# Kernel optimization log

Measured on AMD Instinct MI355X. Metric: run time of the kernel, lower is better.

Reference implementation:

```python
import jax, jax.numpy as jnp
import numpy as np

NQ = 4  # n_qubits_per_head


def _apply_ry(state, theta, q):
    # state: (N, 2,2,2,2) real amplitudes; theta: (N,) per-element angle; wire q
    st = jnp.moveaxis(state, 1 + q, -1)
    c = jnp.cos(0.5 * theta).reshape(-1, 1, 1, 1)
    s = jnp.sin(0.5 * theta).reshape(-1, 1, 1, 1)
    a0, a1 = st[..., 0], st[..., 1]
    st = jnp.stack([c * a0 - s * a1, s * a0 + c * a1], axis=-1)
    return jnp.moveaxis(st, -1, 1 + q)


def _apply_cnot(state, ctrl, tgt):
    st = jnp.moveaxis(state, (1 + ctrl, 1 + tgt), (-2, -1))
    st = jnp.stack([st[..., 0, :], st[..., 1, ::-1]], axis=-2)
    return jnp.moveaxis(st, (-2, -1), (1 + ctrl, 1 + tgt))


def _quantum_circuit(x_in, par):
    # x_in: (N, NQ) data angles; par: (N, L, NQ) variational angles (per head, tiled)
    N = x_in.shape[0]
    L = par.shape[1]
    state = jnp.zeros((N, 2, 2, 2, 2), x_in.dtype).at[:, 0, 0, 0, 0].set(1.0)
    for l in range(L):
        for q in range(NQ):
            state = _apply_ry(state, par[:, l, q], q)
        for q in range(NQ - 1):
            state = _apply_cnot(state, q, q + 1)
        state = _apply_cnot(state, NQ - 1, 0)
    for q in range(NQ):
        state = _apply_ry(state, x_in[:, q], q)
    p = state * state  # probabilities (real amplitudes: only RY/CNOT gates)
    zs = []
    for q in range(NQ):
        st = jnp.moveaxis(p, 1 + q, -1)
        zs.append(jnp.sum(st[..., 0], axis=(1, 2, 3)) - jnp.sum(st[..., 1], axis=(1, 2, 3)))
    return jnp.stack(zs, axis=-1)  # (N, NQ)


def setup_inputs() -> dict:
    key = jax.random.key(0)
    ks = jax.random.split(key, 6)
    B, T, E, H, L = 4, 2048, 1024, 16, 2
    scale = 1.0 / np.sqrt(E)
    x = jax.random.normal(ks[0], (B, T, E), dtype=jnp.float32)
    Wq = jax.random.normal(ks[1], (E, E), dtype=jnp.float32) * scale
    Wk = jax.random.normal(ks[2], (E, E), dtype=jnp.float32) * scale
    Wv = jax.random.normal(ks[3], (E, E), dtype=jnp.float32) * scale
    Wo = jax.random.normal(ks[4], (E, E), dtype=jnp.float32) * scale
    qparams = jax.random.normal(ks[5], (H, L, NQ), dtype=jnp.float32)
    return {"x": x, "Wq": Wq, "Wk": Wk, "Wv": Wv, "Wo": Wo, "qparams": qparams}


def reference(x, Wq, Wk, Wv, Wo, qparams):
    B, T, E = x.shape
    H, L, _ = qparams.shape
    hd = E // H
    q = x @ Wq.T
    k = x @ Wk.T
    v = x @ Wv.T
    # NOTE: original scales by sqrt(embed_dim), not sqrt(head_dim)
    scores = jnp.einsum('bte,bse->bts', q, k) / jnp.sqrt(jnp.asarray(E, x.dtype))
    w = jax.nn.softmax(scores, axis=-1)
    out = jnp.einsum('bts,bse->bte', w, v)
    oh = out.reshape(B, T, H, hd)
    N = B * T * H
    xin = oh[..., :NQ].reshape(N, NQ)
    par = jnp.broadcast_to(qparams[None, None], (B, T, H, L, NQ)).reshape(N, L, NQ)
    z = _quantum_circuit(xin, par)  # (N, NQ)
    zfull = jnp.concatenate([z, jnp.zeros((N, hd - NQ), x.dtype)], axis=-1)
    return zfull.reshape(B, T, E) @ Wo.T
```

## Files before the change

kernel.cpp:

```cpp
#include <hip/hip_runtime.h>
#include <hip/hip_fp16.h>

typedef _Float16 half_t;
typedef __attribute__((ext_vector_type(8))) _Float16 half8;
typedef __attribute__((ext_vector_type(4))) float floatx4;

__device__ __forceinline__ void async_copy16(const void* src, void* dst_lds) {
  __builtin_amdgcn_global_load_lds(
      (__attribute__((address_space(1))) void*)src,
      (__attribute__((address_space(3))) void*)dst_lds, 16, 0, 0);
}

template<int BN, int EPI>
__global__ __launch_bounds__(256) void gemm_nt(
    const half_t* __restrict__ A, const half_t* __restrict__ B,
    void* __restrict__ Cout,
    int lda, int ldb, int ldc, int kIters, int zShift,
    long sAz1, long sBz1, long sCz1,
    long sAz2, long sBz2, long sCz2, float scale,
    const float* __restrict__ qab)
{
  constexpr int BM = 128;
  constexpr int WN = BN / 2;
  constexpr int AN = WN / 16;
  constexpr int RA = BM * 8 / 256;
  constexpr int RB = BN * 8 / 256;
  __shared__ __align__(16) half_t lA[BM * 64];
  __shared__ __align__(16) half_t lB[BN * 64];

  const int tid  = threadIdx.x;
  const int wave = tid >> 6, lane = tid & 63;
  const int wm = wave >> 1, wn = wave & 1;
  const int er = lane >> 4, ec = lane & 15;
  const int sw = ec & 7;

  const long z = blockIdx.z;
  const long z2 = z >> zShift;
  const long z1 = z - (z2 << zShift);
  const half_t* Ab = A + (long)blockIdx.x * BM * lda + z1 * sAz1 + z2 * sAz2;
  const half_t* Bb = B + (long)blockIdx.y * BN * ldb + z1 * sBz1 + z2 * sBz2;
  const long cz = z1 * sCz1 + z2 * sCz2;

  floatx4 acc[4][AN];
  #pragma unroll
  for (int i = 0; i < 4; i++)
    #pragma unroll
    for (int j = 0; j < AN; j++)
      acc[i][j] = (floatx4){0.f, 0.f, 0.f, 0.f};

  for (int ks = 0; ks < kIters; ++ks) {
    const half_t* Ak = Ab + ks * 64;
    const half_t* Bk = Bb + ks * 64;
    #pragma unroll
    for (int r = 0; r < RA; r++) {
      int s = r * 256 + tid;
      int row = s >> 3;
      int kq = (s & 7) ^ (row & 7);
      async_copy16(Ak + (long)row * lda + kq * 8,
                   &lA[(r * 256 + wave * 64) * 8]);
    }
    #pragma unroll
    for (int r = 0; r < RB; r++) {
      int s = r * 256 + tid;
      int row = s >> 3;
      int kq = (s & 7) ^ (row & 7);
      async_copy16(Bk + (long)row * ldb + kq * 8,
                   &lB[(r * 256 + wave * 64) * 8]);
    }
    __syncthreads();

    #pragma unroll
    for (int h = 0; h < 2; h++) {
      half8 af[4], bfv[AN];
      #pragma unroll
      for (int i = 0; i < 4; i++) {
        int row = wm * 64 + i * 16 + ec;
        af[i] = *(const half8*)&lA[row * 64 + (((h * 4 + er) ^ sw) * 8)];
      }
      #pragma unroll
      for (int j = 0; j < AN; j++) {
        int row = wn * WN + j * 16 + ec;
        bfv[j] = *(const half8*)&lB[row * 64 + (((h * 4 + er) ^ sw) * 8)];
      }
      #pragma unroll
      for (int i = 0; i < 4; i++)
        #pragma unroll
        for (int j = 0; j < AN; j++)
          acc[i][j] = __builtin_amdgcn_mfma_f32_16x16x32_f16(
              af[i], bfv[j], acc[i][j], 0, 0, 0);
    }
    __syncthreads();
  }

  const long rowBase = (long)blockIdx.x * BM + wm * 64;
  const long colBase = (long)blockIdx.y * BN + wn * WN;
  #pragma unroll
  for (int i = 0; i < 4; i++)
    #pragma unroll
    for (int j = 0; j < AN; j++)
      #pragma unroll
      for (int r = 0; r < 4; r++) {
        long row = rowBase + i * 16 + er * 4 + r;
        long col = colBase + j * 16 + ec;
        float v = acc[i][j][r];
        if constexpr (EPI == 0) {
          ((half_t*)Cout)[cz + row * (long)ldc + col] = (_Float16)(v * scale);
        } else if constexpr (EPI == 1) {
          ((half_t*)Cout)[cz + col * (long)ldc + row] = (_Float16)v;
        } else if constexpr (EPI == 2) {
          ((float*)Cout)[cz + row * (long)ldc + col] = v * scale;
        } else {
          float za = qab[2 * (int)col], zb = qab[2 * (int)col + 1];
          float zv = za * cosf(v) + zb * sinf(v);
          ((half_t*)Cout)[cz + row * (long)ldc + col] = (_Float16)zv;
        }
      }
}

__global__ __launch_bounds__(256) void softmax_rows(half_t* __restrict__ S,
                                                    int ld)
{
  const long row = blockIdx.x;
  half8* sp = (half8*)(S + row * (long)ld);
  const int t = threadIdx.x;
  const int wave = t >> 6, lane = t & 63;
  half8 hv = sp[t];
  float e[8];
  #pragma unroll
  for (int k = 0; k < 8; k++) e[k] = (float)hv[k];
  float m = e[0];
  #pragma unroll
  for (int k = 1; k < 8; k++) m = fmaxf(m, e[k]);
  #pragma unroll
  for (int o = 32; o > 0; o >>= 1) m = fmaxf(m, __shfl_xor(m, o));
  __shared__ float rmax[4], rsum[4];
  if (lane == 0) rmax[wave] = m;
  __syncthreads();
  m = fmaxf(fmaxf(rmax[0], rmax[1]), fmaxf(rmax[2], rmax[3]));
  float s = 0.f;
  #pragma unroll
  for (int k = 0; k < 8; k++) { e[k] = expf(e[k] - m); s += e[k]; }
  #pragma unroll
  for (int o = 32; o > 0; o >>= 1) s += __shfl_xor(s, o);
  if (lane == 0) rsum[wave] = s;
  __syncthreads();
  float inv = 1.f / (rsum[0] + rsum[1] + rsum[2] + rsum[3]);
  half8 o8;
  #pragma unroll
  for (int k = 0; k < 8; k++) o8[k] = (_Float16)(e[k] * inv);
  sp[t] = o8;
}

__global__ __launch_bounds__(256) void prep_all(
    const float* __restrict__ x,  const float* __restrict__ Wq,
    const float* __restrict__ Wk, const float* __restrict__ Wv,
    const float* __restrict__ Wo, const float* __restrict__ qp, int L,
    half_t* __restrict__ xh, half_t* __restrict__ Wqk,
    half_t* __restrict__ Wv4, half_t* __restrict__ Wos,
    float* __restrict__ qab)
{
  const int bid = blockIdx.x;
  if (bid < 4096) {
    long i = ((long)bid * 256 + threadIdx.x) * 8;
    float4 a = *(const float4*)(x + i);
    float4 b = *(const float4*)(x + i + 4);
    half8 h = {(_Float16)a.x, (_Float16)a.y, (_Float16)a.z, (_Float16)a.w,
               (_Float16)b.x, (_Float16)b.y, (_Float16)b.z, (_Float16)b.w};
    *(half8*)(xh + i) = h;
  } else if (bid < 5120) {
    long i = ((long)(bid - 4096) * 256 + threadIdx.x) * 8;
    int r = (int)(i >> 10);
    int e = (int)(i & 1023);
    const float* src = (r < 1024 ? Wq + (long)r * 1024
                                 : Wk + (long)(r - 1024) * 1024) + e;
    float4 a = *(const float4*)src;
    float4 b = *(const float4*)(src + 4);
    half8 h = {(_Float16)a.x, (_Float16)a.y, (_Float16)a.z, (_Float16)a.w,
               (_Float16)b.x, (_Float16)b.y, (_Float16)b.z, (_Float16)b.w};
    *(half8*)(Wqk + i) = h;
  } else if (bid < 5152) {
    long i = ((long)(bid - 5120) * 256 + threadIdx.x) * 8;
    int c = (int)(i >> 10);
    int e = (int)(i & 1023);
    const float* src = Wv + (long)(((c >> 2) << 6) | (c & 3)) * 1024 + e;
    float4 a = *(const float4*)src;
    float4 b = *(const float4*)(src + 4);
    half8 h = {(_Float16)a.x, (_Float16)a.y, (_Float16)a.z, (_Float16)a.w,
               (_Float16)b.x, (_Float16)b.y, (_Float16)b.z, (_Float16)b.w};
    *(half8*)(Wv4 + i) = h;
  } else if (bid < 5408) {
    int idx = (bid - 5152) * 256 + threadIdx.x;
    int e = idx >> 6, c = idx & 63;
    Wos[idx] = (_Float16)Wo[(long)e * 1024 + (((c >> 2) << 6) | (c & 3))];
  } else {
    int h = threadIdx.x;
    if (h >= 16) return;
    float st[16];
    #pragma unroll
    for (int i = 0; i < 16; i++) st[i] = 0.f;
    st[0] = 1.f;
    for (int l = 0; l < L; l++) {
      #pragma unroll
      for (int q = 0; q < 4; q++) {
        float th = qp[(h * L + l) * 4 + q];
        float c = cosf(0.5f * th), s = sinf(0.5f * th);
        int mq = 8 >> q;
        #pragma unroll
        for (int i = 0; i < 16; i++) {
          if ((i & mq) == 0) {
            float a0 = st[i], a1 = st[i | mq];
            st[i]      = c * a0 - s * a1;
            st[i | mq] = s * a0 + c * a1;
          }
        }
      }
      const int cm[4] = {8, 4, 2, 1};
      const int tm[4] = {4, 2, 1, 8};
      #pragma unroll
      for (int p = 0; p < 4; p++) {
        int mc = cm[p], mt = tm[p];
        #pragma unroll
        for (int i = 0; i < 16; i++) {
          if ((i & mc) != 0 && (i & mt) == 0) {
            float tv = st[i]; st[i] = st[i | mt]; st[i | mt] = tv;
          }
        }
      }
    }
    #pragma unroll
    for (int q = 0; q < 4; q++) {
      int mq = 8 >> q;
      float zc = 0.f, xc = 0.f;
      #pragma unroll
      for (int i = 0; i < 16; i++) {
        float p2 = st[i] * st[i];
        zc += ((i & mq) == 0) ? p2 : -p2;
        if ((i & mq) == 0) xc += st[i] * st[i | mq];
      }
      qab[(h * 4 + q) * 2 + 0] = zc;
      qab[(h * 4 + q) * 2 + 1] = -2.f * xc;
    }
  }
}

extern "C" void kernel_launch(void* const* d_in, const int* in_sizes, int n_in,
                              void* d_out, int out_size, void* d_ws, size_t ws_size,
                              hipStream_t stream)
{
  const float* x  = (const float*)d_in[0];
  const float* Wq = (const float*)d_in[1];
  const float* Wk = (const float*)d_in[2];
  const float* Wv = (const float*)d_in[3];
  const float* Wo = (const float*)d_in[4];
  const float* qp = (const float*)d_in[5];
  const int L = in_sizes[5] / 64;
  float* out = (float*)d_out;

  char* w = (char*)d_ws;
  size_t off = 0;
  auto alloc = [&](size_t bytes) -> void* {
    void* p = w + off;
    off = (off + bytes + 255) & ~(size_t)255;
    return p;
  };
  float*  qab  = (float*)alloc(512);
  half_t* xh   = (half_t*)alloc((size_t)8192 * 1024 * 2);
  half_t* Wqk  = (half_t*)alloc((size_t)2048 * 1024 * 2);
  half_t* Wv4  = (half_t*)alloc((size_t)64 * 1024 * 2);
  half_t* Wos  = (half_t*)alloc((size_t)1024 * 64 * 2);
  half_t* V4th = (half_t*)alloc((size_t)64 * 8192 * 2);
  half_t* Z4   = (half_t*)alloc((size_t)8192 * 64 * 2);

  half_t* QKb = (half_t*)d_out;

  int tier = (ws_size >= off + (size_t)8192 * 2048 * 2 + 256) ? 0 : 1;
  const size_t Sn = (tier == 0) ? (size_t)8192 * 2048 : (size_t)2048 * 2048;
  half_t* S = (half_t*)alloc(Sn * 2);

  prep_all<<<dim3(5409), dim3(256), 0, stream>>>(
      x, Wq, Wk, Wv, Wo, qp, L, xh, Wqk, Wv4, Wos, qab);

  gemm_nt<128, 0><<<dim3(64, 16, 1), 256, 0, stream>>>(
      xh, Wqk, QKb, 1024, 1024, 2048, 16, 0,
      0, 0, 0, 0, 0, 0, 1.f, nullptr);
  gemm_nt<64, 1><<<dim3(64, 1, 1), 256, 0, stream>>>(
      xh, Wv4, V4th, 1024, 1024, 8192, 16, 0,
      0, 0, 0, 0, 0, 0, 1.f, nullptr);

  if (tier == 0) {
    gemm_nt<128, 0><<<dim3(16, 16, 4), 256, 0, stream>>>(
        QKb, QKb + 1024, S, 2048, 2048, 2048, 16, 0,
        0, 0, 0, (long)2048 * 2048, (long)2048 * 2048, (long)2048 * 2048,
        0.03125f, nullptr);
    softmax_rows<<<dim3(8192), dim3(256), 0, stream>>>(S, 2048);
    gemm_nt<64, 5><<<dim3(16, 1, 4), 256, 0, stream>>>(
        S, V4th, Z4, 2048, 8192, 64, 32, 0,
        0, 0, 0, (long)2048 * 2048, 2048, (long)2048 * 64, 1.f, qab);
  } else {
    for (int b = 0; b < 4; b++) {
      const long q0 = (long)b * 2048;
      gemm_nt<128, 0><<<dim3(16, 16, 1), 256, 0, stream>>>(
          QKb + q0 * 2048, QKb + 1024 + q0 * 2048, S,
          2048, 2048, 2048, 16, 0, 0, 0, 0, 0, 0, 0, 0.03125f, nullptr);
      softmax_rows<<<dim3(2048), dim3(256), 0, stream>>>(S, 2048);
      gemm_nt<64, 5><<<dim3(16, 1, 1), 256, 0, stream>>>(
          S, V4th + q0, Z4 + q0 * 64, 2048, 8192, 64, 32, 0,
          0, 0, 0, 0, 0, 0, 1.f, qab);
    }
  }

  gemm_nt<128, 2><<<dim3(64, 8, 1), 256, 0, stream>>>(
      Z4, Wos, out, 64, 64, 1024, 1, 0, 0, 0, 0, 0, 0, 0, 1.f, nullptr);
}
```

Baseline: 263.3 us.

## Add 256x256-tile pipelined GEMM kernel for QK projection and scores

Adds a new 512-thread GEMM kernel with 256x256 output tiles, double-buffered LDS staged through async global-to-LDS copies, and a four-quadrant MFMA schedule that interleaves loads with compute. It replaces the 128x128 GEMM for the fused Q/K projection and for the batched QK^T score matrix. The larger tiles raise arithmetic intensity and data reuse per block. In exchange the grid has fewer blocks, which can leave CUs idle, and register and LDS pressure per block goes up.

```diff
diff --git a/kernel.cpp b/kernel.cpp
--- a/kernel.cpp
+++ b/kernel.cpp
@@ -9,6 +9,164 @@
   __builtin_amdgcn_global_load_lds(
       (__attribute__((address_space(1))) void*)src,
       (__attribute__((address_space(3))) void*)dst_lds, 16, 0, 0);
+}
+
+__global__ __launch_bounds__(512, 2) void gemm_nt_256(
+    const half_t* __restrict__ A, const half_t* __restrict__ B,
+    half_t* __restrict__ C,
+    int lda, int ldb, int ldc, int kIters,
+    long sAz2, long sBz2, long sCz2, float scale)
+{
+  __shared__ __align__(16) half_t sm[2][2][256 * 64];
+
+  const int tid  = threadIdx.x;
+  const int wave = tid >> 6, lane = tid & 63;
+  const int wm = wave >> 2, wn = wave & 3;
+  const int er = lane >> 4, ec = lane & 15;
+  const int sw = ec & 7;
+
+  const long z = blockIdx.z;
+  const half_t* Ab = A + (long)blockIdx.x * 256 * lda + z * sAz2;
+  const half_t* Bb = B + (long)blockIdx.y * 256 * ldb + z * sBz2;
+
+  const int srow = tid >> 3;
+  const int skq  = (tid & 7) ^ (srow & 7);
+
+  floatx4 acc[2][2][4][2];
+  #pragma unroll
+  for (int a = 0; a < 2; a++)
+    #pragma unroll
+    for (int b = 0; b < 2; b++)
+      #pragma unroll
+      for (int i = 0; i < 4; i++)
+        #pragma unroll
+        for (int j = 0; j < 2; j++)
+          acc[a][b][i][j] = (floatx4){0.f, 0.f, 0.f, 0.f};
+
+  half8 af[4][2], bfv[2][2];
+  int cur = 0;
+  const int nt = kIters;
+
+#define STAGE_A(bb, hf, kt) do {                                              \
+    const half_t* Ak_ = Ab + (long)(kt) * 64;                                 \
+    _Pragma("unroll")                                                         \
+    for (int r_ = 0; r_ < 2; r_++) {                                          \
+      int lrow_ = r_ * 64 + srow;                                             \
+      async_copy16(Ak_ + (long)((hf) * 128 + lrow_) * lda + skq * 8,          \
+                   &sm[(bb)][0][(hf) * 8192 + (r_ * 512 + wave * 64) * 8]);   \
+    } } while (0)
+
+#define STAGE_B(bb, hf, kt) do {                                              \
+    const half_t* Bk_ = Bb + (long)(kt) * 64;                                 \
+    _Pragma("unroll")                                                         \
+    for (int r_ = 0; r_ < 2; r_++) {                                          \
+      int lrow_ = r_ * 64 + srow;                                             \
+      async_copy16(Bk_ + (long)((hf) * 128 + lrow_) * ldb + skq * 8,          \
+                   &sm[(bb)][1][(hf) * 8192 + (r_ * 512 + wave * 64) * 8]);   \
+    } } while (0)
+
+#define DS_A(MH) do {                                                         \
+    _Pragma("unroll")                                                         \
+    for (int ii = 0; ii < 4; ii++) {                                          \
+      int row_ = (MH) * 128 + wm * 64 + ii * 16 + ec;                         \
+      _Pragma("unroll")                                                       \
+      for (int ks = 0; ks < 2; ks++)                                          \
+        af[ii][ks] = *(const half8*)                                          \
+            &sm[cur][0][row_ * 64 + (((ks * 4 + er) ^ sw) * 8)];              \
+    } } while (0)
+
+#define DS_B(NH) do {                                                         \
+    _Pragma("unroll")                                                         \
+    for (int jj = 0; jj < 2; jj++) {                                          \
+      int row_ = (NH) * 128 + wn * 32 + jj * 16 + ec;                         \
+      _Pragma("unroll")                                                       \
+      for (int ks = 0; ks < 2; ks++)                                          \
+        bfv[jj][ks] = *(const half8*)                                         \
+            &sm[cur][1][row_ * 64 + (((ks * 4 + er) ^ sw) * 8)];              \
+    } } while (0)
+
+#define MFMA_Q(MH, NH) do {                                                   \
+    __builtin_amdgcn_s_setprio(1);                                            \
+    _Pragma("unroll")                                                         \
+    for (int ks = 0; ks < 2; ks++)                                            \
+      _Pragma("unroll")                                                       \
+      for (int ii = 0; ii < 4; ii++)                                          \
+        _Pragma("unroll")                                                     \
+        for (int jj = 0; jj < 2; jj++)                                        \
+          acc[MH][NH][ii][jj] = __builtin_amdgcn_mfma_f32_16x16x32_f16(       \
+              af[ii][ks], bfv[jj][ks], acc[MH][NH][ii][jj], 0, 0, 0);         \
+    __builtin_amdgcn_s_setprio(0);                                            \
+  } while (0)
+
+#define BAR() __builtin_amdgcn_s_barrier()
+#define LGKM0() asm volatile("s_waitcnt lgkmcnt(0)" ::: "memory")
+#define VMW(N) asm volatile("s_waitcnt vmcnt(" #N ")" ::: "memory")
+
+  STAGE_B(0, 0, 0);
+  STAGE_A(0, 1, 0);
+  STAGE_A(0, 0, 0);
+  STAGE_B(0, 1, 0);
+  if (nt > 1) {
+    STAGE_B(1, 0, 1);
+    STAGE_A(1, 1, 1);
+    VMW(4);
+  } else {
+    VMW(0);
+  }
+  BAR();
+
+  for (int n = 0; n < nt; ++n) {
+    DS_A(0); DS_B(0);
+    if (n + 1 < nt) STAGE_A(cur ^ 1, 0, n + 1);
+    BAR(); LGKM0();
+    MFMA_Q(0, 0);
+    BAR();
+    DS_A(1);
+    if (n + 1 < nt) STAGE_B(cur ^ 1, 1, n + 1);
+    BAR(); LGKM0();
+    MFMA_Q(1, 0);
+    BAR();
+    DS_B(1);
+    if (n + 2 < nt) STAGE_B(cur, 0, n + 2);
+    BAR(); LGKM0();
+    MFMA_Q(1, 1);
+    BAR();
+    DS_A(0);
+    if (n + 2 < nt) STAGE_A(cur, 1, n + 2);
+    VMW(4);
+    BAR(); LGKM0();
+    MFMA_Q(0, 1);
+    BAR();
+    cur ^= 1;
+  }
+
+#undef STAGE_A
+#undef STAGE_B
+#undef DS_A
+#undef DS_B
+#undef MFMA_Q
+#undef BAR
+#undef LGKM0
+#undef VMW
+
+  const long rowBase = (long)blockIdx.x * 256;
+  const long colBase = (long)blockIdx.y * 256;
+  half_t* Cz = C + z * sCz2;
+  #pragma unroll
+  for (int mh = 0; mh < 2; mh++)
+    #pragma unroll
+    for (int nh = 0; nh < 2; nh++)
+      #pragma unroll
+      for (int ii = 0; ii < 4; ii++)
+        #pragma unroll
+        for (int jj = 0; jj < 2; jj++)
+          #pragma unroll
+          for (int r = 0; r < 4; r++) {
+            long row = rowBase + mh * 128 + wm * 64 + ii * 16 + er * 4 + r;
+            long col = colBase + nh * 128 + wn * 32 + jj * 16 + ec;
+            Cz[row * (long)ldc + col] =
+                (_Float16)(acc[mh][nh][ii][jj][r] * scale);
+          }
 }
 
 template<int BN, int EPI>
@@ -280,18 +438,16 @@
   prep_all<<<dim3(5409), dim3(256), 0, stream>>>(
       x, Wq, Wk, Wv, Wo, qp, L, xh, Wqk, Wv4, Wos, qab);
 
-  gemm_nt<128, 0><<<dim3(64, 16, 1), 256, 0, stream>>>(
-      xh, Wqk, QKb, 1024, 1024, 2048, 16, 0,
-      0, 0, 0, 0, 0, 0, 1.f, nullptr);
+  gemm_nt_256<<<dim3(32, 8, 1), 512, 0, stream>>>(
+      xh, Wqk, QKb, 1024, 1024, 2048, 16, 0, 0, 0, 1.f);
   gemm_nt<64, 1><<<dim3(64, 1, 1), 256, 0, stream>>>(
       xh, Wv4, V4th, 1024, 1024, 8192, 16, 0,
       0, 0, 0, 0, 0, 0, 1.f, nullptr);
 
   if (tier == 0) {
-    gemm_nt<128, 0><<<dim3(16, 16, 4), 256, 0, stream>>>(
-        QKb, QKb + 1024, S, 2048, 2048, 2048, 16, 0,
-        0, 0, 0, (long)2048 * 2048, (long)2048 * 2048, (long)2048 * 2048,
-        0.03125f, nullptr);
+    gemm_nt_256<<<dim3(8, 8, 4), 512, 0, stream>>>(
+        QKb, QKb + 1024, S, 2048, 2048, 2048, 16,
+        (long)2048 * 2048, (long)2048 * 2048, (long)2048 * 2048, 0.03125f);
     softmax_rows<<<dim3(8192), dim3(256), 0, stream>>>(S, 2048);
     gemm_nt<64, 5><<<dim3(16, 1, 4), 256, 0, stream>>>(
         S, V4th, Z4, 2048, 8192, 64, 32, 0,
@@ -310,5 +466,6 @@
   }
 
   gemm_nt<128, 2><<<dim3(64, 8, 1), 256, 0, stream>>>(
-      Z4, Wos, out, 64, 64, 1024, 1, 0, 0, 0, 0, 0, 0, 0, 1.f, nullptr);
-}
+      Z4, Wos, out, 64, 64, 1024, 1, 0,
+      0, 0, 0, 0, 0, 0, 1.f, nullptr);
+}
```

Result: faster. 242.0 us (-8.1%).
